# Kernel tuning notes

Measured on AMD Instinct MI355X. Metric: run time of the kernel, lower is better.

Reference implementation:

```python
import jax, jax.numpy as jnp
import numpy as np


def _idct_last(X, norm):
    # IDCT (DCT-III) over the last axis, matching the torch reference exactly.
    N = X.shape[-1]
    Xv = X * 0.5
    if norm == 'ortho':
        scale = jnp.concatenate([
            jnp.full((1,), np.sqrt(N) * 2, dtype=X.dtype),
            jnp.full((N - 1,), np.sqrt(N / 2) * 2, dtype=X.dtype),
        ])
        Xv = Xv * scale
    k = jnp.arange(N, dtype=X.dtype) * (np.pi / (2 * N))
    Wr = jnp.cos(k)
    Wi = jnpp = jnp.sin(k)
    # V_t_i = [0, -Xv reversed (dropping last of the reversed seq)]
    Vti = jnp.concatenate([jnp.zeros_like(Xv[..., :1]), -jnp.flip(Xv, -1)[..., :-1]], axis=-1)
    Vr = Xv * Wr - Vti * Wi
    Vi = Xv * Wi + Vti * Wr
    v = jnp.fft.ifft(jax.lax.complex(Vr, Vi), axis=-1)
    vr = jnp.real(v).astype(X.dtype)
    x = jnp.zeros_like(X)
    x = x.at[..., ::2].set(vr[..., : N - N // 2])
    x = x.at[..., 1::2].set(jnp.flip(vr, -1)[..., : N // 2])
    return x


def _idct_2d(X, norm='ortho'):
    x1 = _idct_last(X, norm)
    x2 = _idct_last(jnp.swapaxes(x1, -1, -2), norm)
    return jnp.swapaxes(x2, -1, -2)


def setup_inputs() -> dict:
    key = jax.random.key(0)
    x = jax.random.normal(key, (16, 32, 256, 256), dtype=jnp.float32)
    return {"x": x}


def reference(x):
    return _idct_2d(x, norm='ortho')
```

## Files before the change

kernel.cpp:

```cpp
#include <hip/hip_runtime.h>
#include <math.h>


constexpr int N = 256;
typedef __attribute__((ext_vector_type(8))) short short8;
typedef __attribute__((ext_vector_type(4))) float f32x4;

constexpr int XS_STRIDE = 40;
constexpr int XS_TILE   = 256 * XS_STRIDE;

__device__ __forceinline__ unsigned short f2bf(float f) {
    unsigned int u = __float_as_uint(f);
    u += 0x7fffu + ((u >> 16) & 1u);
    return (unsigned short)(u >> 16);
}

__device__ __forceinline__ float mvalf(int n, int k) {
    const float CST = 0.006135923151542565f;
    const float W0  = 0.0625f;
    const float WK  = 0.08838834764831845f;
    int q = (k * (2 * n + 1)) & 1023;
    return ((k == 0) ? W0 : WK) * __cosf(CST * (float)q);
}

__global__ __launch_bounds__(256) void mgen(unsigned short* __restrict__ Mg) {
    int idx = blockIdx.x * 256 + threadIdx.x;
    int n = idx >> 8, k = idx & 255;
    Mg[idx] = f2bf(mvalf(n, k));
}

__global__ __launch_bounds__(512, 4) void idct_fused2(
        const float* __restrict__ X,
        const unsigned short* __restrict__ Mg,
        float* __restrict__ Z) {
    __shared__ __align__(16) unsigned char smem[65536];
    unsigned short* Xs0 = (unsigned short*)smem;
    unsigned short* Xs1 = Xs0 + XS_TILE;

    const int bid = blockIdx.x, nb = gridDim.x;
    const int sw = ((nb & 7) == 0) ? ((bid & 7) * (nb >> 3) + (bid >> 3)) : bid;
    const int batch = sw >> 1;
    const int n0 = (sw & 1) << 7;

    const float* Xb = X + (size_t)batch * N * N;
    float*       Zb = Z + (size_t)batch * N * N;

    const int tid = threadIdx.x;
    const int w  = tid >> 6, l = tid & 63;
    const int q  = l >> 4, lr = l & 15;
    const int wi = w >> 1;
    const int wn = w & 1;
    const int srow = tid >> 1, sh = tid & 1;

    const float* xsrc = Xb + (size_t)srow * N + sh * 16;
    const int xoff = srow * XS_STRIDE + sh * 16;

    const unsigned short* mrow0 = Mg + (n0 + wn * 64 +  0 + lr) * N;
    const unsigned short* mrow1 = Mg + (n0 + wn * 64 + 16 + lr) * N;
    const unsigned short* mrow2 = Mg + (n0 + wn * 64 + 32 + lr) * N;
    const unsigned short* mrow3 = Mg + (n0 + wn * 64 + 48 + lr) * N;

    f32x4 acc[4][4];
    #pragma unroll
    for (int r = 0; r < 4; ++r)
        #pragma unroll
        for (int c = 0; c < 4; ++c) acc[r][c] = f32x4{0.f, 0.f, 0.f, 0.f};

    float4 u0, u1, u2, u3;
    {
        const float4* p = (const float4*)xsrc;
        u0 = p[0]; u1 = p[1]; u2 = p[2]; u3 = p[3];
        ushort4 p0 = {f2bf(u0.x), f2bf(u0.y), f2bf(u0.z), f2bf(u0.w)};
        ushort4 p1 = {f2bf(u1.x), f2bf(u1.y), f2bf(u1.z), f2bf(u1.w)};
        ushort4 p2 = {f2bf(u2.x), f2bf(u2.y), f2bf(u2.z), f2bf(u2.w)};
        ushort4 p3 = {f2bf(u3.x), f2bf(u3.y), f2bf(u3.z), f2bf(u3.w)};
        *(ushort4*)&Xs0[xoff + 0]  = p0;
        *(ushort4*)&Xs0[xoff + 4]  = p1;
        *(ushort4*)&Xs0[xoff + 8]  = p2;
        *(ushort4*)&Xs0[xoff + 12] = p3;
    }
    {
        const float4* p = (const float4*)(xsrc + 32);
        u0 = p[0]; u1 = p[1]; u2 = p[2]; u3 = p[3];
    }
    __syncthreads();

    #pragma unroll
    for (int kt = 0; kt < 8; ++kt) {
        unsigned short* xcur = (kt & 1) ? Xs1 : Xs0;
        unsigned short* xnxt = (kt & 1) ? Xs0 : Xs1;

        short8 afr[4], bfr[4];
        #pragma unroll
        for (int r = 0; r < 4; ++r)
            afr[r] = *(const short8*)&xcur[(wi * 64 + r * 16 + lr) * XS_STRIDE + q * 8];
        bfr[0] = *(const short8*)(mrow0 + kt * 32 + q * 8);
        bfr[1] = *(const short8*)(mrow1 + kt * 32 + q * 8);
        bfr[2] = *(const short8*)(mrow2 + kt * 32 + q * 8);
        bfr[3] = *(const short8*)(mrow3 + kt * 32 + q * 8);

        if (kt < 7) {
            ushort4 p0 = {f2bf(u0.x), f2bf(u0.y), f2bf(u0.z), f2bf(u0.w)};
            ushort4 p1 = {f2bf(u1.x), f2bf(u1.y), f2bf(u1.z), f2bf(u1.w)};
            ushort4 p2 = {f2bf(u2.x), f2bf(u2.y), f2bf(u2.z), f2bf(u2.w)};
            ushort4 p3 = {f2bf(u3.x), f2bf(u3.y), f2bf(u3.z), f2bf(u3.w)};
            *(ushort4*)&xnxt[xoff + 0]  = p0;
            *(ushort4*)&xnxt[xoff + 4]  = p1;
            *(ushort4*)&xnxt[xoff + 8]  = p2;
            *(ushort4*)&xnxt[xoff + 12] = p3;
        }
        if (kt < 6) {
            const float4* p = (const float4*)(xsrc + (kt + 2) * 32);
            u0 = p[0]; u1 = p[1]; u2 = p[2]; u3 = p[3];
        }

        __builtin_amdgcn_s_setprio(1);
        #pragma unroll
        for (int r = 0; r < 4; ++r)
            #pragma unroll
            for (int c = 0; c < 4; ++c)
                acc[r][c] = __builtin_amdgcn_mfma_f32_16x16x32_bf16(
                    afr[r], bfr[c], acc[r][c], 0, 0, 0);
        __builtin_amdgcn_s_setprio(0);
        __syncthreads();
    }

    #pragma unroll
    for (int r = 0; r < 4; ++r)
        #pragma unroll
        for (int c = 0; c < 4; ++c) {
            ushort4 pw = {f2bf(acc[r][c][0]), f2bf(acc[r][c][1]),
                          f2bf(acc[r][c][2]), f2bf(acc[r][c][3])};
            int nloc = wn * 64 + c * 16 + lr;
            int i2   = (wi * 64 + r * 16 + q * 4) * 2;
            *(ushort4*)(smem + nloc * 512 + (i2 ^ ((nloc & 7) << 4))) = pw;
        }
    __syncthreads();

    f32x4 acc2[4][4];
    #pragma unroll
    for (int r = 0; r < 4; ++r)
        #pragma unroll
        for (int c = 0; c < 4; ++c) acc2[r][c] = f32x4{0.f, 0.f, 0.f, 0.f};

    const unsigned short* m2row0 = Mg + (wi * 64 +  0 + lr) * N;
    const unsigned short* m2row1 = Mg + (wi * 64 + 16 + lr) * N;
    const unsigned short* m2row2 = Mg + (wi * 64 + 32 + lr) * N;
    const unsigned short* m2row3 = Mg + (wi * 64 + 48 + lr) * N;
    int arow[4], aswz[4];
    #pragma unroll
    for (int r = 0; r < 4; ++r) {
        int nloc = wn * 64 + r * 16 + lr;
        arow[r] = nloc * 512;
        aswz[r] = (nloc & 7) << 4;
    }

    #pragma unroll 2
    for (int it = 0; it < 8; ++it) {
        const int i0 = it * 32;
        short8 af[4], bf[4];
        bf[0] = *(const short8*)(m2row0 + i0 + q * 8);
        bf[1] = *(const short8*)(m2row1 + i0 + q * 8);
        bf[2] = *(const short8*)(m2row2 + i0 + q * 8);
        bf[3] = *(const short8*)(m2row3 + i0 + q * 8);
        #pragma unroll
        for (int r = 0; r < 4; ++r)
            af[r] = *(const short8*)(smem + arow[r] + (((i0 + q * 8) * 2) ^ aswz[r]));
        __builtin_amdgcn_s_setprio(1);
        #pragma unroll
        for (int r = 0; r < 4; ++r)
            #pragma unroll
            for (int c = 0; c < 4; ++c)
                acc2[r][c] = __builtin_amdgcn_mfma_f32_16x16x32_bf16(
                    af[r], bf[c], acc2[r][c], 0, 0, 0);
        __builtin_amdgcn_s_setprio(0);
    }

    #pragma unroll
    for (int r = 0; r < 4; ++r)
        #pragma unroll
        for (int c = 0; c < 4; ++c) {
            float4 v = make_float4(acc2[r][c][0], acc2[r][c][1],
                                   acc2[r][c][2], acc2[r][c][3]);
            int m  = wi * 64 + c * 16 + lr;
            int nn = n0 + wn * 64 + r * 16 + q * 4;
            *(float4*)(Zb + (size_t)m * N + nn) = v;
        }
}

__global__ __launch_bounds__(256) void idct_cols(const float* __restrict__ X,
                                                 float* __restrict__ Y) {
    const int n0 = blockIdx.x * 64;
    const int i0 = blockIdx.y * 64;
    const float* Xb = X + (size_t)blockIdx.z * N * N;
    float* Yb = Y + (size_t)blockIdx.z * N * N;
    __shared__ float Ast[16][68];
    __shared__ float Bs[16][68];
    const int tid = threadIdx.x;
    const int tx = tid & 15, ty = tid >> 4;
    float acc[4][4] = {};
    for (int k0 = 0; k0 < N; k0 += 16) {
        {
            int r = tid >> 2, c4 = (tid & 3) << 2;
            float4 v = *reinterpret_cast<const float4*>(Xb + (size_t)(i0 + r) * N + k0 + c4);
            Ast[c4 + 0][r] = v.x; Ast[c4 + 1][r] = v.y;
            Ast[c4 + 2][r] = v.z; Ast[c4 + 3][r] = v.w;
        }
        #pragma unroll
        for (int j = 0; j < 4; ++j) {
            int ll = tid + 256 * j;
            Bs[ll >> 6][ll & 63] = mvalf(n0 + (ll & 63), k0 + (ll >> 6));
        }
        __syncthreads();
        #pragma unroll
        for (int kk = 0; kk < 16; ++kk) {
            float4 av = *reinterpret_cast<const float4*>(&Ast[kk][ty << 2]);
            float4 bv = *reinterpret_cast<const float4*>(&Bs[kk][tx << 2]);
            float a[4] = {av.x, av.y, av.z, av.w};
            float bb[4] = {bv.x, bv.y, bv.z, bv.w};
            #pragma unroll
            for (int r = 0; r < 4; ++r)
                #pragma unroll
                for (int c = 0; c < 4; ++c) acc[r][c] += a[r] * bb[c];
        }
        __syncthreads();
    }
    #pragma unroll
    for (int r = 0; r < 4; ++r) {
        float4 v = make_float4(acc[r][0], acc[r][1], acc[r][2], acc[r][3]);
        *reinterpret_cast<float4*>(Yb + (size_t)(i0 + (ty << 2) + r) * N + n0 + (tx << 2)) = v;
    }
}

__global__ __launch_bounds__(512) void idct_rows_inplace(float* __restrict__ Y) {
    const int n0 = blockIdx.x * 64;
    float* Yb = Y + (size_t)blockIdx.y * N * N;
    __shared__ float Ys[256][68];
    __shared__ float Ms[16][256];
    const int tid = threadIdx.x;
    #pragma unroll
    for (int j = 0; j < 8; ++j) {
        int ll = tid + 512 * j;
        int row = ll >> 4, c4 = (ll & 15) << 2;
        *reinterpret_cast<float4*>(&Ys[row][c4]) =
            *reinterpret_cast<const float4*>(Yb + (size_t)row * N + n0 + c4);
    }
    __syncthreads();
    const int tx = tid & 15, ty = tid >> 4;
    float acc[8][4] = {};
    for (int i0 = 0; i0 < N; i0 += 16) {
        __syncthreads();
        #pragma unroll
        for (int j = 0; j < 8; ++j) {
            int ll = tid + 512 * j;
            Ms[ll >> 8][ll & 255] = mvalf(ll & 255, i0 + (ll >> 8));
        }
        __syncthreads();
        #pragma unroll
        for (int ii = 0; ii < 16; ++ii) {
            float bb[4];
            #pragma unroll
            for (int c = 0; c < 4; ++c) bb[c] = Ys[i0 + ii][(tx << 2) + c];
            #pragma unroll
            for (int r = 0; r < 8; ++r) {
                float a = Ms[ii][(ty << 3) + r];
                #pragma unroll
                for (int c = 0; c < 4; ++c) acc[r][c] += a * bb[c];
            }
        }
    }
    #pragma unroll
    for (int r = 0; r < 8; ++r) {
        float4 v = make_float4(acc[r][0], acc[r][1], acc[r][2], acc[r][3]);
        *reinterpret_cast<float4*>(Yb + (size_t)((ty << 3) + r) * N + n0 + (tx << 2)) = v;
    }
}

extern "C" void kernel_launch(void* const* d_in, const int* in_sizes, int n_in,
                              void* d_out, int out_size, void* d_ws, size_t ws_size,
                              hipStream_t stream) {
    const float* X = (const float*)d_in[0];
    float* out = (float*)d_out;
    const int total = in_sizes[0];
    const int Bn = total / (N * N);
    const size_t needM = (size_t)N * N * 2;

    if (ws_size >= needM) {
        unsigned short* Mg = (unsigned short*)d_ws;
        mgen<<<N * N / 256, 256, 0, stream>>>(Mg);
        idct_fused2<<<dim3(Bn * 2), 512, 0, stream>>>(X, Mg, out);
    } else {
        idct_cols<<<dim3(N / 64, N / 64, Bn), 256, 0, stream>>>(X, out);
        idct_rows_inplace<<<dim3(N / 64, Bn), 512, 0, stream>>>(out);
    }
}
```

Measured before the change: 285.9 us.

## Load X fragments straight into registers and retile waves as 32-row strips

The first GEMM stage no longer stages the fp32 input through a double-buffered LDS tile with per-step barriers. Each wave now loads its 32 input rows directly from global memory into registers, converts them to bf16 MFMA fragments, and prefetches the next K slice. The wave tiling changes from 4x4 to 2x8 fragments in stage one and 8x2 in stage two, with the B fragments of the constant matrix streamed per MFMA. The aim is to remove the LDS round trip and the barriers in stage one. The cost is less reuse of the constant-matrix loads and global reads that are less coalesced than before.

```diff
diff --git a/kernel.cpp b/kernel.cpp
--- a/kernel.cpp
+++ b/kernel.cpp
@@ -5,14 +5,20 @@
 constexpr int N = 256;
 typedef __attribute__((ext_vector_type(8))) short short8;
 typedef __attribute__((ext_vector_type(4))) float f32x4;
-
-constexpr int XS_STRIDE = 40;
-constexpr int XS_TILE   = 256 * XS_STRIDE;
 
 __device__ __forceinline__ unsigned short f2bf(float f) {
     unsigned int u = __float_as_uint(f);
     u += 0x7fffu + ((u >> 16) & 1u);
     return (unsigned short)(u >> 16);
+}
+
+__device__ __forceinline__ short8 cvt8(float4 a, float4 b) {
+    short8 r;
+    r[0] = (short)f2bf(a.x); r[1] = (short)f2bf(a.y);
+    r[2] = (short)f2bf(a.z); r[3] = (short)f2bf(a.w);
+    r[4] = (short)f2bf(b.x); r[5] = (short)f2bf(b.y);
+    r[6] = (short)f2bf(b.z); r[7] = (short)f2bf(b.w);
+    return r;
 }
 
 __device__ __forceinline__ float mvalf(int n, int k) {
@@ -29,13 +35,11 @@
     Mg[idx] = f2bf(mvalf(n, k));
 }
 
-__global__ __launch_bounds__(512, 4) void idct_fused2(
+__global__ __launch_bounds__(512, 4) void idct_fused3(
         const float* __restrict__ X,
         const unsigned short* __restrict__ Mg,
         float* __restrict__ Z) {
-    __shared__ __align__(16) unsigned char smem[65536];
-    unsigned short* Xs0 = (unsigned short*)smem;
-    unsigned short* Xs1 = Xs0 + XS_TILE;
+    __shared__ __align__(16) unsigned char Wt[65536];
 
     const int bid = blockIdx.x, nb = gridDim.x;
     const int sw = ((nb & 7) == 0) ? ((bid & 7) * (nb >> 3) + (bid >> 3)) : bid;
@@ -48,144 +52,96 @@
     const int tid = threadIdx.x;
     const int w  = tid >> 6, l = tid & 63;
     const int q  = l >> 4, lr = l & 15;
-    const int wi = w >> 1;
-    const int wn = w & 1;
-    const int srow = tid >> 1, sh = tid & 1;
-
-    const float* xsrc = Xb + (size_t)srow * N + sh * 16;
-    const int xoff = srow * XS_STRIDE + sh * 16;
-
-    const unsigned short* mrow0 = Mg + (n0 + wn * 64 +  0 + lr) * N;
-    const unsigned short* mrow1 = Mg + (n0 + wn * 64 + 16 + lr) * N;
-    const unsigned short* mrow2 = Mg + (n0 + wn * 64 + 32 + lr) * N;
-    const unsigned short* mrow3 = Mg + (n0 + wn * 64 + 48 + lr) * N;
-
-    f32x4 acc[4][4];
-    #pragma unroll
-    for (int r = 0; r < 4; ++r)
-        #pragma unroll
-        for (int c = 0; c < 4; ++c) acc[r][c] = f32x4{0.f, 0.f, 0.f, 0.f};
-
-    float4 u0, u1, u2, u3;
-    {
-        const float4* p = (const float4*)xsrc;
-        u0 = p[0]; u1 = p[1]; u2 = p[2]; u3 = p[3];
-        ushort4 p0 = {f2bf(u0.x), f2bf(u0.y), f2bf(u0.z), f2bf(u0.w)};
-        ushort4 p1 = {f2bf(u1.x), f2bf(u1.y), f2bf(u1.z), f2bf(u1.w)};
-        ushort4 p2 = {f2bf(u2.x), f2bf(u2.y), f2bf(u2.z), f2bf(u2.w)};
-        ushort4 p3 = {f2bf(u3.x), f2bf(u3.y), f2bf(u3.z), f2bf(u3.w)};
-        *(ushort4*)&Xs0[xoff + 0]  = p0;
-        *(ushort4*)&Xs0[xoff + 4]  = p1;
-        *(ushort4*)&Xs0[xoff + 8]  = p2;
-        *(ushort4*)&Xs0[xoff + 12] = p3;
-    }
-    {
-        const float4* p = (const float4*)(xsrc + 32);
-        u0 = p[0]; u1 = p[1]; u2 = p[2]; u3 = p[3];
-    }
-    __syncthreads();
-
-    #pragma unroll
+
+    f32x4 acc[2][8];
+    #pragma unroll
+    for (int r = 0; r < 2; ++r)
+        #pragma unroll
+        for (int c = 0; c < 8; ++c) acc[r][c] = f32x4{0.f, 0.f, 0.f, 0.f};
+
+    const float* xr0 = Xb + (size_t)(w * 32 + lr) * N + q * 8;
+    const unsigned short* mb = Mg + (size_t)(n0 + lr) * N + q * 8;
+
+    float4 xa00 = ((const float4*)(xr0 + 0 * N))[0];
+    float4 xa01 = ((const float4*)(xr0 + 0 * N))[1];
+    float4 xa10 = ((const float4*)(xr0 + 16 * N))[0];
+    float4 xa11 = ((const float4*)(xr0 + 16 * N))[1];
+
+    #pragma unroll 1
     for (int kt = 0; kt < 8; ++kt) {
-        unsigned short* xcur = (kt & 1) ? Xs1 : Xs0;
-        unsigned short* xnxt = (kt & 1) ? Xs0 : Xs1;
-
-        short8 afr[4], bfr[4];
-        #pragma unroll
-        for (int r = 0; r < 4; ++r)
-            afr[r] = *(const short8*)&xcur[(wi * 64 + r * 16 + lr) * XS_STRIDE + q * 8];
-        bfr[0] = *(const short8*)(mrow0 + kt * 32 + q * 8);
-        bfr[1] = *(const short8*)(mrow1 + kt * 32 + q * 8);
-        bfr[2] = *(const short8*)(mrow2 + kt * 32 + q * 8);
-        bfr[3] = *(const short8*)(mrow3 + kt * 32 + q * 8);
-
+        short8 afr[2];
+        afr[0] = cvt8(xa00, xa01);
+        afr[1] = cvt8(xa10, xa11);
         if (kt < 7) {
-            ushort4 p0 = {f2bf(u0.x), f2bf(u0.y), f2bf(u0.z), f2bf(u0.w)};
-            ushort4 p1 = {f2bf(u1.x), f2bf(u1.y), f2bf(u1.z), f2bf(u1.w)};
-            ushort4 p2 = {f2bf(u2.x), f2bf(u2.y), f2bf(u2.z), f2bf(u2.w)};
-            ushort4 p3 = {f2bf(u3.x), f2bf(u3.y), f2bf(u3.z), f2bf(u3.w)};
-            *(ushort4*)&xnxt[xoff + 0]  = p0;
-            *(ushort4*)&xnxt[xoff + 4]  = p1;
-            *(ushort4*)&xnxt[xoff + 8]  = p2;
-            *(ushort4*)&xnxt[xoff + 12] = p3;
-        }
-        if (kt < 6) {
-            const float4* p = (const float4*)(xsrc + (kt + 2) * 32);
-            u0 = p[0]; u1 = p[1]; u2 = p[2]; u3 = p[3];
-        }
-
+            const float* nx = xr0 + (kt + 1) * 32;
+            xa00 = ((const float4*)(nx + 0 * N))[0];
+            xa01 = ((const float4*)(nx + 0 * N))[1];
+            xa10 = ((const float4*)(nx + 16 * N))[0];
+            xa11 = ((const float4*)(nx + 16 * N))[1];
+        }
+        const unsigned short* mk = mb + kt * 32;
         __builtin_amdgcn_s_setprio(1);
         #pragma unroll
-        for (int r = 0; r < 4; ++r)
-            #pragma unroll
-            for (int c = 0; c < 4; ++c)
-                acc[r][c] = __builtin_amdgcn_mfma_f32_16x16x32_bf16(
-                    afr[r], bfr[c], acc[r][c], 0, 0, 0);
+        for (int c = 0; c < 8; ++c) {
+            short8 bf = *(const short8*)(mk + c * 16 * N);
+            acc[0][c] = __builtin_amdgcn_mfma_f32_16x16x32_bf16(
+                afr[0], bf, acc[0][c], 0, 0, 0);
+            acc[1][c] = __builtin_amdgcn_mfma_f32_16x16x32_bf16(
+                afr[1], bf, acc[1][c], 0, 0, 0);
+        }
         __builtin_amdgcn_s_setprio(0);
-        __syncthreads();
-    }
-
-    #pragma unroll
-    for (int r = 0; r < 4; ++r)
-        #pragma unroll
-        for (int c = 0; c < 4; ++c) {
+    }
+
+    #pragma unroll
+    for (int r = 0; r < 2; ++r)
+        #pragma unroll
+        for (int c = 0; c < 8; ++c) {
             ushort4 pw = {f2bf(acc[r][c][0]), f2bf(acc[r][c][1]),
                           f2bf(acc[r][c][2]), f2bf(acc[r][c][3])};
-            int nloc = wn * 64 + c * 16 + lr;
-            int i2   = (wi * 64 + r * 16 + q * 4) * 2;
-            *(ushort4*)(smem + nloc * 512 + (i2 ^ ((nloc & 7) << 4))) = pw;
+            int nloc = c * 16 + lr;
+            int i2   = (w * 32 + r * 16 + q * 4) * 2;
+            *(ushort4*)(Wt + nloc * 512 + (i2 ^ ((nloc & 7) << 4))) = pw;
         }
     __syncthreads();
 
-    f32x4 acc2[4][4];
-    #pragma unroll
-    for (int r = 0; r < 4; ++r)
-        #pragma unroll
-        for (int c = 0; c < 4; ++c) acc2[r][c] = f32x4{0.f, 0.f, 0.f, 0.f};
-
-    const unsigned short* m2row0 = Mg + (wi * 64 +  0 + lr) * N;
-    const unsigned short* m2row1 = Mg + (wi * 64 + 16 + lr) * N;
-    const unsigned short* m2row2 = Mg + (wi * 64 + 32 + lr) * N;
-    const unsigned short* m2row3 = Mg + (wi * 64 + 48 + lr) * N;
-    int arow[4], aswz[4];
-    #pragma unroll
-    for (int r = 0; r < 4; ++r) {
-        int nloc = wn * 64 + r * 16 + lr;
-        arow[r] = nloc * 512;
-        aswz[r] = (nloc & 7) << 4;
-    }
+    f32x4 acc2[8][2];
+    #pragma unroll
+    for (int r = 0; r < 8; ++r)
+        #pragma unroll
+        for (int c = 0; c < 2; ++c) acc2[r][c] = f32x4{0.f, 0.f, 0.f, 0.f};
+
+    const unsigned short* m2 = Mg + (size_t)(w * 32 + lr) * N + q * 8;
 
     #pragma unroll 2
     for (int it = 0; it < 8; ++it) {
-        const int i0 = it * 32;
-        short8 af[4], bf[4];
-        bf[0] = *(const short8*)(m2row0 + i0 + q * 8);
-        bf[1] = *(const short8*)(m2row1 + i0 + q * 8);
-        bf[2] = *(const short8*)(m2row2 + i0 + q * 8);
-        bf[3] = *(const short8*)(m2row3 + i0 + q * 8);
-        #pragma unroll
-        for (int r = 0; r < 4; ++r)
-            af[r] = *(const short8*)(smem + arow[r] + (((i0 + q * 8) * 2) ^ aswz[r]));
+        const int ib = it * 32 + q * 8;
+        short8 bf0 = *(const short8*)(m2 + it * 32);
+        short8 bf1 = *(const short8*)(m2 + 16 * N + it * 32);
         __builtin_amdgcn_s_setprio(1);
         #pragma unroll
-        for (int r = 0; r < 4; ++r)
-            #pragma unroll
-            for (int c = 0; c < 4; ++c)
-                acc2[r][c] = __builtin_amdgcn_mfma_f32_16x16x32_bf16(
-                    af[r], bf[c], acc2[r][c], 0, 0, 0);
+        for (int r = 0; r < 8; ++r) {
+            int nloc = r * 16 + lr;
+            short8 af = *(const short8*)(Wt + nloc * 512 +
+                                         ((ib * 2) ^ ((nloc & 7) << 4)));
+            acc2[r][0] = __builtin_amdgcn_mfma_f32_16x16x32_bf16(
+                af, bf0, acc2[r][0], 0, 0, 0);
+            acc2[r][1] = __builtin_amdgcn_mfma_f32_16x16x32_bf16(
+                af, bf1, acc2[r][1], 0, 0, 0);
+        }
         __builtin_amdgcn_s_setprio(0);
     }
 
     #pragma unroll
-    for (int r = 0; r < 4; ++r)
-        #pragma unroll
-        for (int c = 0; c < 4; ++c) {
+    for (int c = 0; c < 2; ++c) {
+        const int m = w * 32 + c * 16 + lr;
+        float* zr = Zb + (size_t)m * N + n0 + q * 4;
+        #pragma unroll
+        for (int r = 0; r < 8; ++r) {
             float4 v = make_float4(acc2[r][c][0], acc2[r][c][1],
                                    acc2[r][c][2], acc2[r][c][3]);
-            int m  = wi * 64 + c * 16 + lr;
-            int nn = n0 + wn * 64 + r * 16 + q * 4;
-            *(float4*)(Zb + (size_t)m * N + nn) = v;
-        }
+            *(float4*)(zr + r * 16) = v;
+        }
+    }
 }
 
 __global__ __launch_bounds__(256) void idct_cols(const float* __restrict__ X,
@@ -288,7 +244,7 @@
     if (ws_size >= needM) {
         unsigned short* Mg = (unsigned short*)d_ws;
         mgen<<<N * N / 256, 256, 0, stream>>>(Mg);
-        idct_fused2<<<dim3(Bn * 2), 512, 0, stream>>>(X, Mg, out);
+        idct_fused3<<<dim3(Bn * 2), 512, 0, stream>>>(X, Mg, out);
     } else {
         idct_cols<<<dim3(N / 64, N / 64, Bn), 256, 0, stream>>>(X, out);
         idct_rows_inplace<<<dim3(N / 64, Bn), 512, 0, stream>>>(out);
```

Result: slower. 293.9 us (+2.8%).
